# Performance work log

Measured on AMD Instinct MI355X. Metric: run time of the kernel, lower is better.

The kernel has to match this reference:

```python
import jax, jax.numpy as jnp
import numpy as np

N = 4096
IN_DIM = 512
NUM_HEADS = 8
SUB_DIM = 64
ETA = 0.5
LAMBDA_SPARSE = 0.1
EDGE_PROB = 0.01


def setup_inputs() -> dict:
    key = jax.random.key(0)
    k_h, k_u, k_a = jax.random.split(key, 3)
    H = jax.random.normal(k_h, (N, IN_DIM), dtype=jnp.float32)
    # Per-head orthonormal subspace bases (QR init, as in the torch module)
    raw = jax.random.normal(k_u, (NUM_HEADS, IN_DIM, SUB_DIM), dtype=jnp.float32)
    U = jax.vmap(lambda a: jnp.linalg.qr(a)[0])(raw)  # [K, in_dim, r]
    # Binary adjacency mask with self-loops (float 0/1)
    adj = (jax.random.uniform(k_a, (N, N)) < EDGE_PROB).astype(jnp.float32)
    adj_mask = jnp.maximum(adj, jnp.eye(N, dtype=jnp.float32))
    threshold = jnp.full((IN_DIM,), LAMBDA_SPARSE, dtype=jnp.float32)
    return {"H": H, "adj_mask": adj_mask, "U": U, "threshold": threshold}


def reference(H, adj_mask, U, threshold):
    r = U.shape[-1]
    scale = jnp.asarray(r, H.dtype) ** 0.5
    # Z_k = U_k^T H^T  -> [K, r, n]
    Z = jnp.einsum('kdr,nd->krn', U, H)
    # scores[k, i, j] = Z_k[:, i] . Z_k[:, j] / sqrt(r), masked to neighbors
    scores = jnp.einsum('kri,krj->kij', Z, Z) / scale
    scores = scores + (1.0 - adj_mask) * (-1e9)
    alpha = jax.nn.softmax(scores, axis=-1)          # [K, n, n]
    # Z_agg[k, :, i] = sum_j alpha[k, i, j] * Z_k[:, j]
    Z_agg = jnp.einsum('krj,kij->kri', Z, alpha)      # [K, r, n]
    # project back and sum heads: [n, d]
    agg = jnp.einsum('kdr,kri->id', U, Z_agg)
    H_half = H + ETA * agg
    H_out = jax.nn.relu(H_half - threshold[None, :])
    # orthogonality loss: sum_{k<l} ||U_k^T U_l||_F^2
    gram = jnp.einsum('kdr,lds->klrs', U, U)
    sq = jnp.sum(gram ** 2, axis=(-1, -2))            # [K, K]
    orth_loss = 0.5 * (jnp.sum(sq) - jnp.trace(sq))
    return H_out, orth_loss
```

## Files before the change

kernel.cpp:

```cpp
#include <hip/hip_runtime.h>
#include <hip/hip_bf16.h>

#define NN   4096
#define DD   512
#define KH   8
#define RR   64
#define CAP  256

typedef unsigned short u16;
typedef unsigned int   u32;
typedef __attribute__((ext_vector_type(8))) short short8;
typedef __attribute__((ext_vector_type(4))) float f32x4;

__device__ __forceinline__ float bflo(u32 v){ union{u32 i; float f;} c; c.i = v << 16;        return c.f; }
__device__ __forceinline__ float bfhi(u32 v){ union{u32 i; float f;} c; c.i = v & 0xFFFF0000u; return c.f; }
__device__ __forceinline__ float bf1(u16 v){ union{u32 i; float f;} c; c.i = ((u32)v) << 16;  return c.f; }
__device__ __forceinline__ u16 f2bf(float f){ __hip_bfloat16 h = __float2bfloat16(f); return *reinterpret_cast<u16*>(&h); }

__global__ __launch_bounds__(256) void prep_all(const float* __restrict__ H, const float* __restrict__ U,
                                                u16* __restrict__ Hb, u16* __restrict__ Bt1,
                                                u16* __restrict__ Bt2, float* __restrict__ lossA) {
    __shared__ float tile[64][65];
    int b = blockIdx.x, t = threadIdx.x;
    if (b < 2048) {
        size_t id = (size_t)b * 256 + t;
        float4 v = *(const float4*)(H + id * 4);
        ushort4 o; o.x = f2bf(v.x); o.y = f2bf(v.y); o.z = f2bf(v.z); o.w = f2bf(v.w);
        *(ushort4*)(Hb + id * 4) = o;
        return;
    }
    if (b == 2112) { if (t == 0) lossA[0] = 0.f; return; }
    int b2 = b - 2048;
    int k = b2 >> 3, d0 = (b2 & 7) * 64;
    #pragma unroll
    for (int s = 0; s < 4; s++) {
        int u = t + 256 * s;
        int dd = u >> 4, rq = u & 15;
        float4 v = *(const float4*)(U + ((size_t)(k * DD + d0 + dd)) * RR + rq * 4);
        tile[dd][rq * 4 + 0] = v.x; tile[dd][rq * 4 + 1] = v.y;
        tile[dd][rq * 4 + 2] = v.z; tile[dd][rq * 4 + 3] = v.w;
    }
    __syncthreads();
    {
        int r = t >> 2;
        #pragma unroll
        for (int ii = 0; ii < 16; ii++) {
            int dd = (t & 3) * 16 + ii;
            Bt1[(size_t)(k * RR + r) * DD + d0 + dd] = f2bf(tile[dd][r]);
        }
    }
    {
        int dd = t >> 2, rb = (t & 3) * 16;
        #pragma unroll
        for (int ii = 0; ii < 16; ii++) {
            Bt2[(size_t)(d0 + dd) * DD + k * RR + rb + ii] = f2bf(tile[dd][rb + ii]);
        }
    }
}

__global__ __launch_bounds__(256) void zgemm_mfma(const u16* __restrict__ Hb, const u16* __restrict__ Bt1,
                                                  u16* __restrict__ Zb) {
    __shared__ short As[64][40];
    __shared__ short Bs[64][40];
    const int t = threadIdx.x;
    const int i0 = blockIdx.x * 64, n0 = blockIdx.y * 64;
    const int w = t >> 6, lane = t & 63;
    const int lm = lane & 15, lg = lane >> 4;
    f32x4 acc[4] = {};
    for (int kc = 0; kc < DD; kc += 32) {
        {   int row = t >> 2, g = t & 3;
            *(short8*)&As[row][g * 8] = *(const short8*)(Hb  + (size_t)(i0 + row) * DD + kc + g * 8);
            *(short8*)&Bs[row][g * 8] = *(const short8*)(Bt1 + (size_t)(n0 + row) * DD + kc + g * 8);
        }
        __syncthreads();
        short8 af = *(const short8*)&As[w * 16 + lm][lg * 8];
        #pragma unroll
        for (int b = 0; b < 4; b++) {
            short8 bfr = *(const short8*)&Bs[b * 16 + lm][lg * 8];
            acc[b] = __builtin_amdgcn_mfma_f32_16x16x32_bf16(af, bfr, acc[b], 0, 0, 0);
        }
        __syncthreads();
    }
    #pragma unroll
    for (int b = 0; b < 4; b++)
        #pragma unroll
        for (int q = 0; q < 4; q++) {
            int row = i0 + w * 16 + lg * 4 + q;
            int col = n0 + b * 16 + lm;
            Zb[(size_t)row * DD + col] = f2bf(acc[b][q]);
        }
}

__global__ __launch_bounds__(512) void attn3(const u16* __restrict__ Zb, const float* __restrict__ adj,
                                             u16* __restrict__ Zaggb) {
    const int i = blockIdx.x, t = threadIdx.x;
    const int k = t >> 6, lane = t & 63;
    __shared__ int   nbrS[CAP];
    __shared__ int   cntS;
    __shared__ float ziS[DD];
    __shared__ short zbuf[KH][16][72];
    __shared__ float wS[KH][16];
    if (t == 0) cntS = 0;
    __syncthreads();
    const float* arow = adj + (size_t)i * NN;
    #pragma unroll
    for (int qq = 0; qq < 2; qq++) {
        int j = (qq * 512 + t) * 4;
        float4 mv = *(const float4*)(arow + j);
        if (mv.x != 0.f) { int p = atomicAdd(&cntS, 1); if (p < CAP) nbrS[p] = j;     }
        if (mv.y != 0.f) { int p = atomicAdd(&cntS, 1); if (p < CAP) nbrS[p] = j + 1; }
        if (mv.z != 0.f) { int p = atomicAdd(&cntS, 1); if (p < CAP) nbrS[p] = j + 2; }
        if (mv.w != 0.f) { int p = atomicAdd(&cntS, 1); if (p < CAP) nbrS[p] = j + 3; }
    }
    if (t < 256) {
        u32 v = *(const u32*)(Zb + (size_t)i * DD + t * 2);
        ziS[t * 2] = bflo(v); ziS[t * 2 + 1] = bfhi(v);
    }
    __syncthreads();
    const int ci = min(cntS, CAP);

    const int q = lane & 3, nl = lane >> 2;
    const float* zik = ziS + k * 64 + q * 16;
    float m = -3.0e38f, l = 0.f, acc = 0.f;
    const int nchunk = (ci + 15) >> 4;
    for (int ch = 0; ch < nchunk; ch++) {
        const int base = ch * 16;
        const int cact = min(16, ci - base);
        const int j = nbrS[base + ((nl < cact) ? nl : 0)];
        const uint4* zp = (const uint4*)(Zb + (size_t)j * DD + k * 64 + q * 16);
        uint4 v0 = zp[0], v1 = zp[1];
        float s = bflo(v0.x) * zik[0]  + bfhi(v0.x) * zik[1]
                + bflo(v0.y) * zik[2]  + bfhi(v0.y) * zik[3]
                + bflo(v0.z) * zik[4]  + bfhi(v0.z) * zik[5]
                + bflo(v0.w) * zik[6]  + bfhi(v0.w) * zik[7]
                + bflo(v1.x) * zik[8]  + bfhi(v1.x) * zik[9]
                + bflo(v1.y) * zik[10] + bfhi(v1.y) * zik[11]
                + bflo(v1.z) * zik[12] + bfhi(v1.z) * zik[13]
                + bflo(v1.w) * zik[14] + bfhi(v1.w) * zik[15];
        *(uint4*)&zbuf[k][nl][q * 16]     = v0;
        *(uint4*)&zbuf[k][nl][q * 16 + 8] = v1;
        s += __shfl_xor(s, 1); s += __shfl_xor(s, 2);
        s *= 0.125f;
        if (nl >= cact) s = -3.0e38f;
        float mx = s;
        #pragma unroll
        for (int off = 4; off < 64; off <<= 1) mx = fmaxf(mx, __shfl_xor(mx, off));
        const float mnew = fmaxf(m, mx);
        const float scale = __expf(m - mnew);
        const float e = (nl < cact) ? __expf(s - mnew) : 0.f;
        float se = e;
        #pragma unroll
        for (int off = 4; off < 64; off <<= 1) se += __shfl_xor(se, off);
        l = l * scale + se;
        m = mnew;
        acc *= scale;
        if (q == 0) wS[k][nl] = e;
        for (int c = 0; c < cact; c++)
            acc += wS[k][c] * bf1(zbuf[k][c][lane]);
    }
    Zaggb[(size_t)i * DD + k * 64 + lane] = f2bf(acc / l);
}

__global__ __launch_bounds__(256) void outgemm_mfma(const u16* __restrict__ Ab, const u16* __restrict__ Btb,
                                                    const float* __restrict__ H, const float* __restrict__ thr,
                                                    float* __restrict__ out) {
    __shared__ short As[64][40];
    __shared__ short Bs[64][40];
    const int t = threadIdx.x;
    const int i0 = blockIdx.x * 64, n0 = blockIdx.y * 64;
    const int w = t >> 6, lane = t & 63;
    const int lm = lane & 15, lg = lane >> 4;
    f32x4 acc[4] = {};
    for (int kc = 0; kc < DD; kc += 32) {
        {   int row = t >> 2, g = t & 3;
            *(short8*)&As[row][g * 8] = *(const short8*)(Ab  + (size_t)(i0 + row) * DD + kc + g * 8);
            *(short8*)&Bs[row][g * 8] = *(const short8*)(Btb + (size_t)(n0 + row) * DD + kc + g * 8);
        }
        __syncthreads();
        short8 af = *(const short8*)&As[w * 16 + lm][lg * 8];
        #pragma unroll
        for (int b = 0; b < 4; b++) {
            short8 bfr = *(const short8*)&Bs[b * 16 + lm][lg * 8];
            acc[b] = __builtin_amdgcn_mfma_f32_16x16x32_bf16(af, bfr, acc[b], 0, 0, 0);
        }
        __syncthreads();
    }
    #pragma unroll
    for (int b = 0; b < 4; b++) {
        const int col = n0 + b * 16 + lm;
        const float th = thr[col];
        #pragma unroll
        for (int q = 0; q < 4; q++) {
            int row = i0 + w * 16 + lg * 4 + q;
            float h = H[(size_t)row * DD + col];
            out[(size_t)row * DD + col] = fmaxf(h + 0.5f * acc[b][q] - th, 0.f);
        }
    }
}

__global__ __launch_bounds__(256) void orth_kernel(const float* __restrict__ U, float* __restrict__ loss) {
    int pb = blockIdx.x >> 4;
    int stile = blockIdx.x & 15;
    int idx = pb, k = 0, l = 1;
    for (int kk = 0; kk < 8; kk++) {
        int c = 7 - kk;
        if (idx < c) { k = kk; l = kk + 1 + idx; break; }
        idx -= c;
    }
    int t = threadIdx.x;
    int r = t & 63;
    int s = stile * 4 + (t >> 6);
    const float* Uk = U + (size_t)k * DD * RR;
    const float* Ul = U + (size_t)l * DD * RR;
    float acc = 0.f;
    for (int d = 0; d < DD; d++) {
        acc += Uk[d * RR + r] * Ul[d * RR + s];
    }
    float v = acc * acc;
    #pragma unroll
    for (int off = 32; off; off >>= 1) v += __shfl_down(v, off, 64);
    __shared__ float red[4];
    if ((t & 63) == 0) red[t >> 6] = v;
    __syncthreads();
    if (t == 0) atomicAdd(loss, red[0] + red[1] + red[2] + red[3]);
}

__global__ void loss_fin_kernel(const float* __restrict__ lossf, float* __restrict__ out) {
    out[0] = lossf[0];
}

extern "C" void kernel_launch(void* const* d_in, const int* in_sizes, int n_in,
                              void* d_out, int out_size, void* d_ws, size_t ws_size,
                              hipStream_t stream) {
    const float* H   = (const float*)d_in[0];
    const float* adj = (const float*)d_in[1];
    const float* U   = (const float*)d_in[2];
    const float* thr = (const float*)d_in[3];
    float* out = (float*)d_out;

    char* ws = (char*)d_ws;
    float* lossA = (float*)ws;
    u16*   Hb    = (u16*)(ws + 1024);
    u16*   Zb    = (u16*)(ws + 1024 + 4u  * 1024 * 1024);
    u16*   Zaggb = (u16*)(ws + 1024 + 8u  * 1024 * 1024);
    u16*   Bt1   = (u16*)(ws + 1024 + 12u * 1024 * 1024);
    u16*   Bt2   = (u16*)(ws + 1024 + 12u * 1024 * 1024 + 512u * 1024);

    prep_all<<<2113, 256, 0, stream>>>(H, U, Hb, Bt1, Bt2, lossA);
    zgemm_mfma<<<dim3(64, 8), 256, 0, stream>>>(Hb, Bt1, Zb);
    attn3<<<NN, 512, 0, stream>>>(Zb, adj, Zaggb);
    outgemm_mfma<<<dim3(64, 8), 256, 0, stream>>>(Zaggb, Bt2, H, thr, out);
    orth_kernel<<<28 * 16, 256, 0, stream>>>(U, lossA);
    loss_fin_kernel<<<1, 1, 0, stream>>>(lossA, out + (size_t)NN * DD);
}
```

Before: 180.4 us.

## Fuse H bf16 cast into Z GEMM, rework attention, tile orth loss

Removes the separate H-to-bf16 conversion pass by converting fp32 H inside the Z GEMM tile load. Both GEMMs now use a K-chunk of 64 per sync. The attention kernel computes one neighbor score per lane across 64 neighbors and gathers Z rows directly from global memory instead of staging through shared memory. The orthogonality loss uses shared-memory tiled blocks, and a done-counter in the last block replaces the separate finalize kernel. The trade-off is more global gathers in the attention accumulate loop, plus reliance on atomic ordering for the loss write.

After: 213.1 us. 18.2% more time.

```diff
diff --git a/kernel.cpp b/kernel.cpp
--- a/kernel.cpp
+++ b/kernel.cpp
@@ -14,24 +14,15 @@
 
 __device__ __forceinline__ float bflo(u32 v){ union{u32 i; float f;} c; c.i = v << 16;        return c.f; }
 __device__ __forceinline__ float bfhi(u32 v){ union{u32 i; float f;} c; c.i = v & 0xFFFF0000u; return c.f; }
-__device__ __forceinline__ float bf1(u16 v){ union{u32 i; float f;} c; c.i = ((u32)v) << 16;  return c.f; }
 __device__ __forceinline__ u16 f2bf(float f){ __hip_bfloat16 h = __float2bfloat16(f); return *reinterpret_cast<u16*>(&h); }
 
-__global__ __launch_bounds__(256) void prep_all(const float* __restrict__ H, const float* __restrict__ U,
-                                                u16* __restrict__ Hb, u16* __restrict__ Bt1,
-                                                u16* __restrict__ Bt2, float* __restrict__ lossA) {
+__global__ __launch_bounds__(256) void prep_u(const float* __restrict__ U, u16* __restrict__ Bt1,
+                                              u16* __restrict__ Bt2, float* __restrict__ lossA,
+                                              int* __restrict__ doneA) {
     __shared__ float tile[64][65];
     int b = blockIdx.x, t = threadIdx.x;
-    if (b < 2048) {
-        size_t id = (size_t)b * 256 + t;
-        float4 v = *(const float4*)(H + id * 4);
-        ushort4 o; o.x = f2bf(v.x); o.y = f2bf(v.y); o.z = f2bf(v.z); o.w = f2bf(v.w);
-        *(ushort4*)(Hb + id * 4) = o;
-        return;
-    }
-    if (b == 2112) { if (t == 0) lossA[0] = 0.f; return; }
-    int b2 = b - 2048;
-    int k = b2 >> 3, d0 = (b2 & 7) * 64;
+    if (b == 64) { if (t == 0) { lossA[0] = 0.f; doneA[0] = 0; } return; }
+    int k = b >> 3, d0 = (b & 7) * 64;
     #pragma unroll
     for (int s = 0; s < 4; s++) {
         int u = t + 256 * s;
@@ -58,26 +49,36 @@
     }
 }
 
-__global__ __launch_bounds__(256) void zgemm_mfma(const u16* __restrict__ Hb, const u16* __restrict__ Bt1,
+__global__ __launch_bounds__(256) void zgemm_mfma(const float* __restrict__ H, const u16* __restrict__ Bt1,
                                                   u16* __restrict__ Zb) {
-    __shared__ short As[64][40];
-    __shared__ short Bs[64][40];
+    __shared__ short As[64][72];
+    __shared__ short Bs[64][72];
     const int t = threadIdx.x;
     const int i0 = blockIdx.x * 64, n0 = blockIdx.y * 64;
     const int w = t >> 6, lane = t & 63;
     const int lm = lane & 15, lg = lane >> 4;
     f32x4 acc[4] = {};
-    for (int kc = 0; kc < DD; kc += 32) {
-        {   int row = t >> 2, g = t & 3;
-            *(short8*)&As[row][g * 8] = *(const short8*)(Hb  + (size_t)(i0 + row) * DD + kc + g * 8);
+    for (int kc = 0; kc < DD; kc += 64) {
+        #pragma unroll
+        for (int s = 0; s < 2; s++) {
+            int c = t + 256 * s; int row = c >> 3, g = c & 7;
+            float4 p0 = *(const float4*)(H + (size_t)(i0 + row) * DD + kc + g * 8);
+            float4 p1 = *(const float4*)(H + (size_t)(i0 + row) * DD + kc + g * 8 + 4);
+            short8 av;
+            av[0]=f2bf(p0.x); av[1]=f2bf(p0.y); av[2]=f2bf(p0.z); av[3]=f2bf(p0.w);
+            av[4]=f2bf(p1.x); av[5]=f2bf(p1.y); av[6]=f2bf(p1.z); av[7]=f2bf(p1.w);
+            *(short8*)&As[row][g * 8] = av;
             *(short8*)&Bs[row][g * 8] = *(const short8*)(Bt1 + (size_t)(n0 + row) * DD + kc + g * 8);
         }
         __syncthreads();
-        short8 af = *(const short8*)&As[w * 16 + lm][lg * 8];
-        #pragma unroll
-        for (int b = 0; b < 4; b++) {
-            short8 bfr = *(const short8*)&Bs[b * 16 + lm][lg * 8];
-            acc[b] = __builtin_amdgcn_mfma_f32_16x16x32_bf16(af, bfr, acc[b], 0, 0, 0);
+        #pragma unroll
+        for (int ks = 0; ks < 64; ks += 32) {
+            short8 af = *(const short8*)&As[w * 16 + lm][ks + lg * 8];
+            #pragma unroll
+            for (int b = 0; b < 4; b++) {
+                short8 bfr = *(const short8*)&Bs[b * 16 + lm][ks + lg * 8];
+                acc[b] = __builtin_amdgcn_mfma_f32_16x16x32_bf16(af, bfr, acc[b], 0, 0, 0);
+            }
         }
         __syncthreads();
     }
@@ -91,15 +92,14 @@
         }
 }
 
-__global__ __launch_bounds__(512) void attn3(const u16* __restrict__ Zb, const float* __restrict__ adj,
+__global__ __launch_bounds__(512) void attn4(const u16* __restrict__ Zb, const float* __restrict__ adj,
                                              u16* __restrict__ Zaggb) {
     const int i = blockIdx.x, t = threadIdx.x;
     const int k = t >> 6, lane = t & 63;
-    __shared__ int   nbrS[CAP];
+    __shared__ int   nbrS[CAP + 64];
     __shared__ int   cntS;
     __shared__ float ziS[DD];
-    __shared__ short zbuf[KH][16][72];
-    __shared__ float wS[KH][16];
+    __shared__ float wS[KH][64];
     if (t == 0) cntS = 0;
     __syncthreads();
     const float* arow = adj + (size_t)i * NN;
@@ -118,70 +118,85 @@
     }
     __syncthreads();
     const int ci = min(cntS, CAP);
-
-    const int q = lane & 3, nl = lane >> 2;
-    const float* zik = ziS + k * 64 + q * 16;
-    float m = -3.0e38f, l = 0.f, acc = 0.f;
-    const int nchunk = (ci + 15) >> 4;
-    for (int ch = 0; ch < nchunk; ch++) {
-        const int base = ch * 16;
-        const int cact = min(16, ci - base);
-        const int j = nbrS[base + ((nl < cact) ? nl : 0)];
-        const uint4* zp = (const uint4*)(Zb + (size_t)j * DD + k * 64 + q * 16);
-        uint4 v0 = zp[0], v1 = zp[1];
-        float s = bflo(v0.x) * zik[0]  + bfhi(v0.x) * zik[1]
-                + bflo(v0.y) * zik[2]  + bfhi(v0.y) * zik[3]
-                + bflo(v0.z) * zik[4]  + bfhi(v0.z) * zik[5]
-                + bflo(v0.w) * zik[6]  + bfhi(v0.w) * zik[7]
-                + bflo(v1.x) * zik[8]  + bfhi(v1.x) * zik[9]
-                + bflo(v1.y) * zik[10] + bfhi(v1.y) * zik[11]
-                + bflo(v1.z) * zik[12] + bfhi(v1.z) * zik[13]
-                + bflo(v1.w) * zik[14] + bfhi(v1.w) * zik[15];
-        *(uint4*)&zbuf[k][nl][q * 16]     = v0;
-        *(uint4*)&zbuf[k][nl][q * 16 + 8] = v1;
-        s += __shfl_xor(s, 1); s += __shfl_xor(s, 2);
+    if (t < 64) nbrS[ci + t] = nbrS[0];
+    __syncthreads();
+
+    const int half = lane >> 5, L = lane & 31;
+    float m = -3.0e38f, l = 0.f;
+    float accA = 0.f, accB = 0.f;
+    const float4* zik4 = (const float4*)(ziS + k * 64);
+    for (int base = 0; base < ci; base += 64) {
+        const int cact = min(64, ci - base);
+        const int j = nbrS[base + lane];
+        const uint4* zp = (const uint4*)(Zb + (size_t)j * DD + k * 64);
+        float s = 0.f;
+        #pragma unroll
+        for (int q = 0; q < 8; q++) {
+            uint4 v = zp[q];
+            float4 a0 = zik4[q * 2], a1 = zik4[q * 2 + 1];
+            s += bflo(v.x) * a0.x + bfhi(v.x) * a0.y
+               + bflo(v.y) * a0.z + bfhi(v.y) * a0.w
+               + bflo(v.z) * a1.x + bfhi(v.z) * a1.y
+               + bflo(v.w) * a1.z + bfhi(v.w) * a1.w;
+        }
         s *= 0.125f;
-        if (nl >= cact) s = -3.0e38f;
+        if (lane >= cact) s = -3.0e38f;
         float mx = s;
         #pragma unroll
-        for (int off = 4; off < 64; off <<= 1) mx = fmaxf(mx, __shfl_xor(mx, off));
+        for (int off = 1; off < 64; off <<= 1) mx = fmaxf(mx, __shfl_xor(mx, off));
         const float mnew = fmaxf(m, mx);
         const float scale = __expf(m - mnew);
-        const float e = (nl < cact) ? __expf(s - mnew) : 0.f;
+        const float e = (lane < cact) ? __expf(s - mnew) : 0.f;
         float se = e;
         #pragma unroll
-        for (int off = 4; off < 64; off <<= 1) se += __shfl_xor(se, off);
+        for (int off = 1; off < 64; off <<= 1) se += __shfl_xor(se, off);
         l = l * scale + se;
         m = mnew;
-        acc *= scale;
-        if (q == 0) wS[k][nl] = e;
-        for (int c = 0; c < cact; c++)
-            acc += wS[k][c] * bf1(zbuf[k][c][lane]);
-    }
-    Zaggb[(size_t)i * DD + k * 64 + lane] = f2bf(acc / l);
+        accA *= scale; accB *= scale;
+        wS[k][lane] = e;
+        for (int cc = 0; cc < cact; cc += 2) {
+            const float wgt = wS[k][cc + half];
+            const int  jc  = nbrS[base + cc + half];
+            u32 z2 = *(const u32*)(Zb + (size_t)jc * DD + k * 64 + 2 * L);
+            accA += wgt * bflo(z2);
+            accB += wgt * bfhi(z2);
+        }
+    }
+    accA += __shfl_xor(accA, 32);
+    accB += __shfl_xor(accB, 32);
+    const float inv = 1.0f / l;
+    if (lane < 32) {
+        u32 o = ((u32)f2bf(accA * inv)) | (((u32)f2bf(accB * inv)) << 16);
+        *(u32*)(Zaggb + (size_t)i * DD + k * 64 + 2 * L) = o;
+    }
 }
 
 __global__ __launch_bounds__(256) void outgemm_mfma(const u16* __restrict__ Ab, const u16* __restrict__ Btb,
                                                     const float* __restrict__ H, const float* __restrict__ thr,
                                                     float* __restrict__ out) {
-    __shared__ short As[64][40];
-    __shared__ short Bs[64][40];
+    __shared__ short As[64][72];
+    __shared__ short Bs[64][72];
     const int t = threadIdx.x;
     const int i0 = blockIdx.x * 64, n0 = blockIdx.y * 64;
     const int w = t >> 6, lane = t & 63;
     const int lm = lane & 15, lg = lane >> 4;
     f32x4 acc[4] = {};
-    for (int kc = 0; kc < DD; kc += 32) {
-        {   int row = t >> 2, g = t & 3;
+    for (int kc = 0; kc < DD; kc += 64) {
+        #pragma unroll
+        for (int s = 0; s < 2; s++) {
+            int c = t + 256 * s; int row = c >> 3, g = c & 7;
             *(short8*)&As[row][g * 8] = *(const short8*)(Ab  + (size_t)(i0 + row) * DD + kc + g * 8);
             *(short8*)&Bs[row][g * 8] = *(const short8*)(Btb + (size_t)(n0 + row) * DD + kc + g * 8);
         }
         __syncthreads();
-        short8 af = *(const short8*)&As[w * 16 + lm][lg * 8];
-        #pragma unroll
-        for (int b = 0; b < 4; b++) {
-            short8 bfr = *(const short8*)&Bs[b * 16 + lm][lg * 8];
-            acc[b] = __builtin_amdgcn_mfma_f32_16x16x32_bf16(af, bfr, acc[b], 0, 0, 0);
+        #pragma unroll
+        for (int ks = 0; ks < 64; ks += 32) {
+            short8 af = *(const short8*)&As[w * 16 + lm][ks + lg * 8];
+            #pragma unroll
+            for (int b = 0; b < 4; b++) {
+                short8 bfr = *(const short8*)&Bs[b * 16 + lm][ks + lg * 8];
+                acc[b] = __builtin_amdgcn_mfma_f32_16x16x32_bf16(af, bfr, acc[b], 0, 0, 0);
+            }
         }
         __syncthreads();
     }
@@ -198,35 +213,60 @@
     }
 }
 
-__global__ __launch_bounds__(256) void orth_kernel(const float* __restrict__ U, float* __restrict__ loss) {
-    int pb = blockIdx.x >> 4;
-    int stile = blockIdx.x & 15;
-    int idx = pb, k = 0, l = 1;
+__global__ __launch_bounds__(256) void orth_kernel(const float* __restrict__ U, float* __restrict__ loss,
+                                                   int* __restrict__ done, float* __restrict__ outLoss) {
+    __shared__ float UkT[64][20];
+    __shared__ float UlT[64][68];
+    const int pb = blockIdx.x >> 2, strip = blockIdx.x & 3;
+    int idx = pb, k = 0, lh = 1;
+    #pragma unroll
     for (int kk = 0; kk < 8; kk++) {
         int c = 7 - kk;
-        if (idx < c) { k = kk; l = kk + 1 + idx; break; }
+        if (idx < c) { k = kk; lh = kk + 1 + idx; break; }
         idx -= c;
     }
-    int t = threadIdx.x;
-    int r = t & 63;
-    int s = stile * 4 + (t >> 6);
-    const float* Uk = U + (size_t)k * DD * RR;
-    const float* Ul = U + (size_t)l * DD * RR;
-    float acc = 0.f;
-    for (int d = 0; d < DD; d++) {
-        acc += Uk[d * RR + r] * Ul[d * RR + s];
-    }
-    float v = acc * acc;
+    const int t = threadIdx.x;
+    const int r = t & 15;
+    const int s0 = (t >> 4) * 4;
+    const int r0g = strip * 16;
+    const float* Uk = U + (size_t)k  * DD * RR;
+    const float* Ul = U + (size_t)lh * DD * RR;
+    float a0 = 0.f, a1 = 0.f, a2 = 0.f, a3 = 0.f;
+    for (int dc = 0; dc < DD; dc += 64) {
+        {
+            int dd = t >> 2, rq = t & 3;
+            *(float4*)&UkT[dd][rq * 4] = *(const float4*)(Uk + (size_t)(dc + dd) * RR + r0g + rq * 4);
+        }
+        #pragma unroll
+        for (int s = 0; s < 4; s++) {
+            int u = t + 256 * s;
+            int dd = u >> 4, sq = u & 15;
+            *(float4*)&UlT[dd][sq * 4] = *(const float4*)(Ul + (size_t)(dc + dd) * RR + sq * 4);
+        }
+        __syncthreads();
+        #pragma unroll 4
+        for (int dd = 0; dd < 64; dd++) {
+            float a = UkT[dd][r];
+            float4 b = *(const float4*)&UlT[dd][s0];
+            a0 += a * b.x; a1 += a * b.y; a2 += a * b.z; a3 += a * b.w;
+        }
+        __syncthreads();
+    }
+    float v = a0 * a0 + a1 * a1 + a2 * a2 + a3 * a3;
     #pragma unroll
     for (int off = 32; off; off >>= 1) v += __shfl_down(v, off, 64);
     __shared__ float red[4];
     if ((t & 63) == 0) red[t >> 6] = v;
     __syncthreads();
-    if (t == 0) atomicAdd(loss, red[0] + red[1] + red[2] + red[3]);
-}
-
-__global__ void loss_fin_kernel(const float* __restrict__ lossf, float* __restrict__ out) {
-    out[0] = lossf[0];
+    if (t == 0) {
+        atomicAdd(loss, red[0] + red[1] + red[2] + red[3]);
+        __threadfence();
+        int d = atomicAdd(done, 1);
+        if (d == 111) {
+            float total = atomicAdd(loss, 0.f);
+            outLoss[0] = total;
+        }
+    }
 }
 
 extern "C" void kernel_launch(void* const* d_in, const int* in_sizes, int n_in,
@@ -240,16 +280,15 @@
 
     char* ws = (char*)d_ws;
     float* lossA = (float*)ws;
-    u16*   Hb    = (u16*)(ws + 1024);
-    u16*   Zb    = (u16*)(ws + 1024 + 4u  * 1024 * 1024);
-    u16*   Zaggb = (u16*)(ws + 1024 + 8u  * 1024 * 1024);
-    u16*   Bt1   = (u16*)(ws + 1024 + 12u * 1024 * 1024);
-    u16*   Bt2   = (u16*)(ws + 1024 + 12u * 1024 * 1024 + 512u * 1024);
-
-    prep_all<<<2113, 256, 0, stream>>>(H, U, Hb, Bt1, Bt2, lossA);
-    zgemm_mfma<<<dim3(64, 8), 256, 0, stream>>>(Hb, Bt1, Zb);
-    attn3<<<NN, 512, 0, stream>>>(Zb, adj, Zaggb);
+    int*   doneA = (int*)(ws + 64);
+    u16*   Zb    = (u16*)(ws + 1024);
+    u16*   Zaggb = (u16*)(ws + 1024 + 4u * 1024 * 1024);
+    u16*   Bt1   = (u16*)(ws + 1024 + 8u * 1024 * 1024);
+    u16*   Bt2   = (u16*)(ws + 1024 + 8u * 1024 * 1024 + 512u * 1024);
+
+    prep_u<<<65, 256, 0, stream>>>(U, Bt1, Bt2, lossA, doneA);
+    zgemm_mfma<<<dim3(64, 8), 256, 0, stream>>>(H, Bt1, Zb);
+    attn4<<<NN, 512, 0, stream>>>(Zb, adj, Zaggb);
     outgemm_mfma<<<dim3(64, 8), 256, 0, stream>>>(Zaggb, Bt2, H, thr, out);
-    orth_kernel<<<28 * 16, 256, 0, stream>>>(U, lossA);
-    loss_fin_kernel<<<1, 1, 0, stream>>>(lossA, out + (size_t)NN * DD);
-}
+    orth_kernel<<<112, 256, 0, stream>>>(U, lossA, doneA, out + (size_t)NN * DD);
+}
```
